# Kernel tuning notes

Measured on AMD Instinct MI355X. Metric: run time of the kernel, lower is better.

Reference implementation:

```python
import jax, jax.numpy as jnp
import numpy as np
from jax import lax

B, C, L = 2048, 9605, 8
WL_PER_LABEL = 50
ALPHA = 0.5        # training_config['alpha4']
ALPHA1 = 0.1       # margin
ALPHA2 = 2.0       # training_config['alpha2']
ALPHA3 = 10.0      # training_config['alpha3']
ALPHA_OTHER = 0.5
NEG = jnp.float32(-1e30)


def setup_inputs() -> dict:
    key = jax.random.key(0)
    k1, k2, k3, k4 = jax.random.split(key, 4)
    x = jax.random.normal(k1, (B, C), dtype=jnp.float32) * 2.0
    y = (jax.random.uniform(k2, (B, C)) < 0.005).astype(jnp.float32)
    y_neg = (jax.random.uniform(k3, (B, C)) < 0.005).astype(jnp.float32)
    # whitelist masks: L app-labels, each whitelisting ~WL_PER_LABEL raw classes
    idx = jax.random.randint(k4, (L, WL_PER_LABEL), 0, C)
    wl_masks = jnp.zeros((L, C), dtype=bool).at[jnp.arange(L)[:, None], idx].set(True)
    return {"x": x, "y": y, "y_neg": y_neg, "wl_masks": wl_masks}


def reference(x, y, y_neg, wl_masks):
    # y_neg is consumed by the original forward (find_gt_whitelist) but never
    # affects the returned loss, faithfully ignored here.
    xs_pos = jax.nn.sigmoid(x)                                  # [B, C]
    # top_k_thres = max(11th-largest sigmoid, alpha_other)
    thres = jnp.maximum(lax.top_k(xs_pos, 11)[0][:, 10], ALPHA_OTHER)  # [B]
    # per-label whitelist max: m[b,l] = max_{c in wl_l} xs_pos[b,c]
    m = jnp.max(jnp.where(wl_masks[None, :, :], xs_pos[:, None, :], NEG), axis=-1)  # [B, L]
    # label l is a ground-truth whitelist label iff y has any positive in wl_l
    has_pos = jnp.einsum('bc,lc->bl', y, wl_masks.astype(y.dtype)) > 0   # [B, L]
    correct_max = jnp.max(jnp.where(has_pos, m, NEG), axis=-1)           # [B]
    incorrect_max = jnp.max(jnp.where(~has_pos, m, NEG), axis=-1)        # [B]
    any_correct = jnp.any(has_pos, axis=-1)
    any_incorrect = jnp.any(~has_pos, axis=-1)
    # union whitelist max (the "other" branch uses xs_pos over all wl indices)
    union_max = jnp.max(jnp.where(jnp.any(wl_masks, axis=0)[None, :], xs_pos, NEG), axis=-1)
    x1 = jnp.where(any_correct, correct_max, thres)
    x2 = jnp.where(any_correct,
                   jnp.where(any_incorrect, jnp.maximum(incorrect_max, thres), thres),
                   union_max)
    coef = jnp.where(any_correct, 1.0, 1.0 - ALPHA)
    d = x2 - x1 + ALPHA1
    rank = jnp.where(d > 0, ALPHA2, 1.0) * jax.nn.sigmoid(ALPHA3 * d)
    return jnp.mean(coef * rank)
```

## Files before the change

kernel.cpp:

```cpp
#include <hip/hip_runtime.h>

#define CC 9605
#define BB 2048
#define LL 8
#define CAND_MAX 384
#define NEGF (-1e30f)

#define WS_PARTIALS_OFF 16384

__device__ __forceinline__ unsigned enc_f(float f) {
  unsigned u = __float_as_uint(f);
  return (u & 0x80000000u) ? ~u : (u | 0x80000000u);
}
__device__ __forceinline__ float dec_u(unsigned e) {
  unsigned u = (e & 0x80000000u) ? (e & 0x7fffffffu) : ~e;
  return __uint_as_float(u);
}
__device__ __forceinline__ float sigm(float z) {
  return 1.0f / (1.0f + __expf(-z));
}

__global__ void wl_sniff(const unsigned* __restrict__ wlw,
                         unsigned* __restrict__ wsu) {
  const int nwords = (LL * CC) / 4;
  const int stride = gridDim.x * blockDim.x;
  unsigned f = 0u;
  for (int j = blockIdx.x * blockDim.x + threadIdx.x; j < nwords; j += stride) {
    unsigned w = wlw[j];
#pragma unroll
    for (int k = 0; k < 4; ++k) {
      unsigned b = (w >> (8 * k)) & 255u;
      if (b == 1u)    { f |= 2u; if (k != 0) f |= 1u; }
      if (b == 0x3fu) { f |= 8u; if (k == 1) f |= 4u; }
    }
  }
#pragma unroll
  for (int off = 32; off >= 1; off >>= 1) f |= __shfl_xor(f, off, 64);
  if ((threadIdx.x & 63) == 0 && f) atomicOr(&wsu[1], f);
}

__global__ void wl_compact(const unsigned char* __restrict__ wl,
                           unsigned* __restrict__ wsu) {
  const int tid = threadIdx.x;
  const int lane = tid & 63;
  const int c = blockIdx.x * 256 + tid;
  const unsigned g = wsu[1];
  const int dt = (g & 1u) ? 0 : (g & 4u) ? 3 : (g & 2u) ? 1 : (g & 8u) ? 2 : 0;
  const int* wl32 = (const int*)wl;
  const float* wlf = (const float*)wl;
  const unsigned short* wlh = (const unsigned short*)wl;
  unsigned m = 0u;
  if (c < CC) {
#pragma unroll
    for (int l = 0; l < LL; ++l) {
      int j = l * CC + c;
      bool on;
      if (dt == 0) on = (wl[j] != 0);
      else if (dt == 1) on = (wl32[j] != 0);
      else if (dt == 2) on = (wlf[j] != 0.0f);
      else on = (wlh[j] != 0);
      if (on) m |= (1u << l);
    }
  }
  unsigned long long bal = __ballot(m != 0u);
  if (bal) {
    unsigned wcnt = (unsigned)__popcll(bal);
    unsigned basep = 0u;
    if (lane == 0) basep = atomicAdd(&wsu[0], wcnt);
    basep = __shfl(basep, 0, 64);
    if (m) {
      unsigned pos = basep + (unsigned)__popcll(bal & ((1ull << lane) - 1ull));
      if (pos < 2048u) wsu[4 + pos] = ((unsigned)c << 8) | m;
    }
  }
}

__global__ __launch_bounds__(256, 4) void loss_kernel(
    const float* __restrict__ x, const float* __restrict__ y,
    const unsigned* __restrict__ wsu, float* __restrict__ partials) {
  __shared__ __align__(16) unsigned sh_row[9608];
  __shared__ unsigned sh_cand[CAND_MAX];
  __shared__ unsigned sh_redM[4];
  __shared__ unsigned sh_redC[4];
  __shared__ unsigned sh_cnt;
  __shared__ unsigned sh_e11;
  __shared__ float sh_wl[4][10];

  const int tid = threadIdx.x;
  const int lane = tid & 63;
  const int wid = tid >> 6;
  const int b = blockIdx.x;
  const long long base = (long long)b * CC;

  const int soff = (4 - (b & 3)) & 3;
  const int ngroups = (CC - soff) >> 2;
  const int tailn = CC - soff - (ngroups << 2);
  const int m_extra = soff + tailn;
  const float4* vp = (const float4*)(x + base + soff);
  float4 t[10];
#pragma unroll
  for (int i = 0; i < 9; ++i) t[i] = vp[tid + (i << 8)];
  const int g9 = tid + (9 << 8);
  if (g9 < ngroups) t[9] = vp[g9];
  else { t[9].x = NEGF; t[9].y = NEGF; t[9].z = NEGF; t[9].w = NEGF; }
  float tailv = NEGF;
  int tailcol = 0;
  if (tid < m_extra) {
    tailcol = (tid < soff) ? tid : (soff + (ngroups << 2) + (tid - soff));
    tailv = x[base + tailcol];
  }

  const unsigned nu = wsu[0];
  const unsigned* ents = wsu + 4;
  unsigned ent0 = 0u, ent1 = 0u;
  float gx0 = NEGF, gy0 = 0.0f, gx1 = NEGF, gy1 = 0.0f;
  const bool h0 = (unsigned)tid < nu;
  const bool h1 = (unsigned)(tid + 256) < nu;
  if (h0) ent0 = ents[tid];
  if (h1) ent1 = ents[tid + 256];
  if (h0) { gx0 = x[base + (ent0 >> 8)]; gy0 = y[base + (ent0 >> 8)]; }
  if (h1) { gx1 = x[base + (ent1 >> 8)]; gy1 = y[base + (ent1 >> 8)]; }

  uint4* rv = (uint4*)sh_row;
  unsigned mx = 0u;
#pragma unroll
  for (int i = 0; i < 10; ++i) {
    int g = tid + (i << 8);
    uint4 e;
    e.x = enc_f(t[i].x); e.y = enc_f(t[i].y);
    e.z = enc_f(t[i].z); e.w = enc_f(t[i].w);
    if (i < 9 || g < ngroups) {
      mx = max(mx, max(max(e.x, e.y), max(e.z, e.w)));
      rv[g] = e;
    }
  }
  if (tid < m_extra) {
    unsigned e = enc_f(tailv);
    mx = max(mx, e);
    sh_row[(ngroups << 2) + tid] = e;
  }
  if (tid < 3) sh_row[9605 + tid] = 0u;
  if (tid == 0) sh_cnt = 0u;

#pragma unroll
  for (int off = 32; off >= 1; off >>= 1) mx = max(mx, __shfl_xor(mx, off, 64));
  if (lane == 0) sh_redM[wid] = mx;
  __syncthreads();
  const unsigned Emax =
      max(max(sh_redM[0], sh_redM[1]), max(sh_redM[2], sh_redM[3]));

  auto blk_count = [&](unsigned T) -> unsigned {
    unsigned cnt = 0u;
#pragma unroll
    for (int i = 0; i < 10; ++i) {
      int g = tid + (i << 8);
      if (g < 2402) {
        uint4 v = rv[g];
        cnt += (v.x >= T) + (v.y >= T) + (v.z >= T) + (v.w >= T);
      }
    }
#pragma unroll
    for (int off = 32; off >= 1; off >>= 1) cnt += __shfl_xor(cnt, off, 64);
    __syncthreads();
    if (lane == 0) sh_redC[wid] = cnt;
    __syncthreads();
    return sh_redC[0] + sh_redC[1] + sh_redC[2] + sh_redC[3];
  };

  unsigned E11 = 0u;
  bool done = false;
  unsigned lo = (Emax > (1u << 23)) ? (Emax - (1u << 23)) : 1u;
  unsigned hi = Emax + 1u;
  unsigned c = blk_count(lo);
  while (c < 11u && lo > 1u) {
    hi = lo;
    lo = (lo > (1u << 23)) ? (lo - (1u << 23)) : 1u;
    c = blk_count(lo);
  }
  while (c > CAND_MAX) {
    if (hi - lo <= 1u) { E11 = lo; done = true; break; }
    unsigned mid = lo + ((hi - lo) >> 1);
    unsigned cm = blk_count(mid);
    if (cm >= 11u) { lo = mid; c = cm; } else { hi = mid; }
  }

  if (!done) {
#pragma unroll
    for (int i = 0; i < 10; ++i) {
      int g = tid + (i << 8);
      uint4 v;
      if (g < 2402) v = rv[g];
      else { v.x = 0u; v.y = 0u; v.z = 0u; v.w = 0u; }
      unsigned vals[4] = {v.x, v.y, v.z, v.w};
#pragma unroll
      for (int k = 0; k < 4; ++k) {
        bool pr = (vals[k] >= lo);
        unsigned long long bal = __ballot(pr);
        if (bal) {
          unsigned wcnt = (unsigned)__popcll(bal);
          unsigned basep = 0u;
          if (lane == 0) basep = atomicAdd(&sh_cnt, wcnt);
          basep = __shfl(basep, 0, 64);
          if (pr) {
            unsigned posn =
                basep + (unsigned)__popcll(bal & ((1ull << lane) - 1ull));
            sh_cand[posn] = vals[k];
          }
        }
      }
    }
    __syncthreads();

    if (wid == 0) {
      unsigned v0[6];
#pragma unroll
      for (int j = 0; j < 6; ++j) {
        unsigned idx = (unsigned)lane + 64u * j;
        v0[j] = (idx < c) ? sh_cand[idx] : 0u;
      }
      unsigned ans = 0u;
      for (int r = 0; r < 11; ++r) {
        unsigned lmx = v0[0];
#pragma unroll
        for (int j = 1; j < 6; ++j) lmx = max(lmx, v0[j]);
        unsigned wm = lmx;
#pragma unroll
        for (int off = 32; off >= 1; off >>= 1)
          wm = max(wm, __shfl_xor(wm, off, 64));
        ans = wm;
        if (r < 10) {
          unsigned long long bal = __ballot(lmx == wm);
          int first = (int)__ffsll((long long)bal) - 1;
          if (lane == first) {
            bool rm = false;
#pragma unroll
            for (int j = 0; j < 6; ++j) {
              if (!rm && v0[j] == wm) { v0[j] = 0u; rm = true; }
            }
          }
        }
      }
      if (lane == 0) sh_e11 = ans;
    }
    __syncthreads();
    E11 = sh_e11;
  }

  float lm[8];
#pragma unroll
  for (int l = 0; l < 8; ++l) lm[l] = NEGF;
  unsigned pmask = 0u;
  if (h0) {
    unsigned mk = ent0 & 255u;
    pmask |= mk;
    if (gy0 > 0.0f) pmask |= (mk << 8);
#pragma unroll
    for (int l = 0; l < 8; ++l)
      if ((mk >> l) & 1u) lm[l] = fmaxf(lm[l], gx0);
  }
  if (h1) {
    unsigned mk = ent1 & 255u;
    pmask |= mk;
    if (gy1 > 0.0f) pmask |= (mk << 8);
#pragma unroll
    for (int l = 0; l < 8; ++l)
      if ((mk >> l) & 1u) lm[l] = fmaxf(lm[l], gx1);
  }
  for (unsigned e = (unsigned)tid + 512u; e < nu; e += 256u) {
    unsigned ent = ents[e];
    unsigned mk = ent & 255u;
    float xv = x[base + (ent >> 8)];
    float yv = y[base + (ent >> 8)];
    pmask |= mk;
    if (yv > 0.0f) pmask |= (mk << 8);
#pragma unroll
    for (int l = 0; l < 8; ++l)
      if ((mk >> l) & 1u) lm[l] = fmaxf(lm[l], xv);
  }
#pragma unroll
  for (int off = 32; off >= 1; off >>= 1) {
    pmask |= __shfl_xor(pmask, off, 64);
#pragma unroll
    for (int l = 0; l < 8; ++l) lm[l] = fmaxf(lm[l], __shfl_xor(lm[l], off, 64));
  }
  if (lane == 0) {
#pragma unroll
    for (int l = 0; l < 8; ++l) sh_wl[wid][l] = lm[l];
    sh_wl[wid][8] = __uint_as_float(pmask);
  }
  __syncthreads();

  if (tid == 0) {
    float LM[8];
    unsigned PM = 0u;
#pragma unroll
    for (int l = 0; l < 8; ++l) LM[l] = NEGF;
    for (int w = 0; w < 4; ++w) {
#pragma unroll
      for (int l = 0; l < 8; ++l) LM[l] = fmaxf(LM[l], sh_wl[w][l]);
      PM |= __float_as_uint(sh_wl[w][8]);
    }
    unsigned PR = PM & 255u, PO = (PM >> 8) & 255u;
    float thres = fmaxf(sigm(dec_u(E11)), 0.5f);
    float cmax = NEGF, imax = NEGF, umax = NEGF;
#pragma unroll
    for (int l = 0; l < 8; ++l) {
      if ((PR >> l) & 1u) {
        float ml = sigm(LM[l]);
        umax = fmaxf(umax, ml);
        if ((PO >> l) & 1u) cmax = fmaxf(cmax, ml);
        else imax = fmaxf(imax, ml);
      }
    }
    bool anyc = (PO != 0u);
    bool anyi = (PO != 255u);
    float x1 = anyc ? cmax : thres;
    float x2 = anyc ? (anyi ? fmaxf(imax, thres) : thres)
                    : ((nu > 0u) ? umax : NEGF);
    float coef = anyc ? 1.0f : 0.5f;
    float dd = x2 - x1 + 0.1f;
    float rank = ((dd > 0.0f) ? 2.0f : 1.0f) * sigm(10.0f * dd);
    partials[b] = coef * rank;
  }
}

__global__ void final_reduce(const float* __restrict__ partials,
                             float* __restrict__ out) {
  __shared__ float sh[4];
  const int tid = threadIdx.x;
  const int lane = tid & 63;
  const int wid = tid >> 6;
  float s = 0.0f;
  for (int i = tid; i < BB; i += 256) s += partials[i];
#pragma unroll
  for (int off = 32; off >= 1; off >>= 1) s += __shfl_xor(s, off, 64);
  if (lane == 0) sh[wid] = s;
  __syncthreads();
  if (tid == 0) out[0] = (sh[0] + sh[1] + sh[2] + sh[3]) * (1.0f / (float)BB);
}

extern "C" void kernel_launch(void* const* d_in, const int* in_sizes, int n_in,
                              void* d_out, int out_size, void* d_ws,
                              size_t ws_size, hipStream_t stream) {
  const float* x = (const float*)d_in[0];
  const float* y = (const float*)d_in[1];
  const unsigned char* wl = (const unsigned char*)d_in[3];
  float* out = (float*)d_out;
  unsigned* wsu = (unsigned*)d_ws;
  float* partials = (float*)((char*)d_ws + WS_PARTIALS_OFF);

  hipMemsetAsync(d_ws, 0, 16, stream);
  wl_sniff<<<64, 256, 0, stream>>>((const unsigned*)wl, wsu);
  wl_compact<<<(CC + 255) / 256, 256, 0, stream>>>(wl, wsu);
  loss_kernel<<<BB, 256, 0, stream>>>(x, y, wsu, partials);
  final_reduce<<<1, 256, 0, stream>>>(partials, out);
}
```

Baseline: 232.0 us.

## Keep row in registers with 1024-thread blocks instead of shared-memory staging

The loss kernel moves from 256 to 1024 threads per block, and each thread now holds 13 encoded values of the row in registers. The 38 KB shared-memory row buffer and the repeated LDS scans in each threshold-count pass are gone. The coarse search step is halved, which narrows the first window in exchange for possibly more expansion passes. Block-wide reductions now span 16 waves, so each count pass pays for more synchronisation across more waves.

```diff
diff --git a/kernel.cpp b/kernel.cpp
--- a/kernel.cpp
+++ b/kernel.cpp
@@ -3,6 +3,8 @@
 #define CC 9605
 #define BB 2048
 #define LL 8
+#define TPB 1024
+#define NWAVE 16
 #define CAND_MAX 384
 #define NEGF (-1e30f)
 
@@ -75,16 +77,15 @@
   }
 }
 
-__global__ __launch_bounds__(256, 4) void loss_kernel(
+__global__ __launch_bounds__(TPB) void loss_kernel(
     const float* __restrict__ x, const float* __restrict__ y,
     const unsigned* __restrict__ wsu, float* __restrict__ partials) {
-  __shared__ __align__(16) unsigned sh_row[9608];
   __shared__ unsigned sh_cand[CAND_MAX];
-  __shared__ unsigned sh_redM[4];
-  __shared__ unsigned sh_redC[4];
+  __shared__ unsigned sh_redM[NWAVE];
+  __shared__ unsigned sh_redC[NWAVE];
   __shared__ unsigned sh_cnt;
   __shared__ unsigned sh_e11;
-  __shared__ float sh_wl[4][10];
+  __shared__ float sh_wl[NWAVE][9];
 
   const int tid = threadIdx.x;
   const int lane = tid & 63;
@@ -97,84 +98,78 @@
   const int tailn = CC - soff - (ngroups << 2);
   const int m_extra = soff + tailn;
   const float4* vp = (const float4*)(x + base + soff);
-  float4 t[10];
-#pragma unroll
-  for (int i = 0; i < 9; ++i) t[i] = vp[tid + (i << 8)];
-  const int g9 = tid + (9 << 8);
-  if (g9 < ngroups) t[9] = vp[g9];
-  else { t[9].x = NEGF; t[9].y = NEGF; t[9].z = NEGF; t[9].w = NEGF; }
-  float tailv = NEGF;
-  int tailcol = 0;
+  const float4 t0 = vp[tid];
+  const float4 t1 = vp[tid + 1024];
+  const int g2 = tid + 2048;
+  const bool hg2 = (g2 < ngroups);
+  float4 t2;
+  if (hg2) t2 = vp[g2];
+  float tailv = 0.0f;
   if (tid < m_extra) {
-    tailcol = (tid < soff) ? tid : (soff + (ngroups << 2) + (tid - soff));
-    tailv = x[base + tailcol];
+    int col = (tid < soff) ? tid : (soff + (ngroups << 2) + (tid - soff));
+    tailv = x[base + col];
   }
 
   const unsigned nu = wsu[0];
   const unsigned* ents = wsu + 4;
-  unsigned ent0 = 0u, ent1 = 0u;
-  float gx0 = NEGF, gy0 = 0.0f, gx1 = NEGF, gy1 = 0.0f;
   const bool h0 = (unsigned)tid < nu;
-  const bool h1 = (unsigned)(tid + 256) < nu;
-  if (h0) ent0 = ents[tid];
-  if (h1) ent1 = ents[tid + 256];
-  if (h0) { gx0 = x[base + (ent0 >> 8)]; gy0 = y[base + (ent0 >> 8)]; }
-  if (h1) { gx1 = x[base + (ent1 >> 8)]; gy1 = y[base + (ent1 >> 8)]; }
-
-  uint4* rv = (uint4*)sh_row;
+  unsigned ent0 = 0u;
+  float gx0 = NEGF, gy0 = 0.0f;
+  if (h0) {
+    ent0 = ents[tid];
+    gx0 = x[base + (ent0 >> 8)];
+    gy0 = y[base + (ent0 >> 8)];
+  }
+
+  unsigned enc[13];
+  enc[0] = enc_f(t0.x); enc[1] = enc_f(t0.y);
+  enc[2] = enc_f(t0.z); enc[3] = enc_f(t0.w);
+  enc[4] = enc_f(t1.x); enc[5] = enc_f(t1.y);
+  enc[6] = enc_f(t1.z); enc[7] = enc_f(t1.w);
+  if (hg2) {
+    enc[8] = enc_f(t2.x); enc[9] = enc_f(t2.y);
+    enc[10] = enc_f(t2.z); enc[11] = enc_f(t2.w);
+  } else {
+    enc[8] = 0u; enc[9] = 0u; enc[10] = 0u; enc[11] = 0u;
+  }
+  enc[12] = (tid < m_extra) ? enc_f(tailv) : 0u;
+  if (tid == 0) sh_cnt = 0u;
+
   unsigned mx = 0u;
 #pragma unroll
-  for (int i = 0; i < 10; ++i) {
-    int g = tid + (i << 8);
-    uint4 e;
-    e.x = enc_f(t[i].x); e.y = enc_f(t[i].y);
-    e.z = enc_f(t[i].z); e.w = enc_f(t[i].w);
-    if (i < 9 || g < ngroups) {
-      mx = max(mx, max(max(e.x, e.y), max(e.z, e.w)));
-      rv[g] = e;
-    }
-  }
-  if (tid < m_extra) {
-    unsigned e = enc_f(tailv);
-    mx = max(mx, e);
-    sh_row[(ngroups << 2) + tid] = e;
-  }
-  if (tid < 3) sh_row[9605 + tid] = 0u;
-  if (tid == 0) sh_cnt = 0u;
-
+  for (int i = 0; i < 13; ++i) mx = max(mx, enc[i]);
 #pragma unroll
   for (int off = 32; off >= 1; off >>= 1) mx = max(mx, __shfl_xor(mx, off, 64));
   if (lane == 0) sh_redM[wid] = mx;
   __syncthreads();
-  const unsigned Emax =
-      max(max(sh_redM[0], sh_redM[1]), max(sh_redM[2], sh_redM[3]));
+  unsigned Emax = 0u;
+#pragma unroll
+  for (int w = 0; w < NWAVE; ++w) Emax = max(Emax, sh_redM[w]);
 
   auto blk_count = [&](unsigned T) -> unsigned {
     unsigned cnt = 0u;
 #pragma unroll
-    for (int i = 0; i < 10; ++i) {
-      int g = tid + (i << 8);
-      if (g < 2402) {
-        uint4 v = rv[g];
-        cnt += (v.x >= T) + (v.y >= T) + (v.z >= T) + (v.w >= T);
-      }
-    }
+    for (int i = 0; i < 13; ++i) cnt += (enc[i] >= T) ? 1u : 0u;
 #pragma unroll
     for (int off = 32; off >= 1; off >>= 1) cnt += __shfl_xor(cnt, off, 64);
     __syncthreads();
     if (lane == 0) sh_redC[wid] = cnt;
     __syncthreads();
-    return sh_redC[0] + sh_redC[1] + sh_redC[2] + sh_redC[3];
+    unsigned s = 0u;
+#pragma unroll
+    for (int w = 0; w < NWAVE; ++w) s += sh_redC[w];
+    return s;
   };
 
+  const unsigned STEP = 1u << 22;
   unsigned E11 = 0u;
   bool done = false;
-  unsigned lo = (Emax > (1u << 23)) ? (Emax - (1u << 23)) : 1u;
+  unsigned lo = (Emax > STEP) ? (Emax - STEP) : 1u;
   unsigned hi = Emax + 1u;
   unsigned c = blk_count(lo);
   while (c < 11u && lo > 1u) {
     hi = lo;
-    lo = (lo > (1u << 23)) ? (lo - (1u << 23)) : 1u;
+    lo = (lo > STEP) ? (lo - STEP) : 1u;
     c = blk_count(lo);
   }
   while (c > CAND_MAX) {
@@ -186,26 +181,18 @@
 
   if (!done) {
 #pragma unroll
-    for (int i = 0; i < 10; ++i) {
-      int g = tid + (i << 8);
-      uint4 v;
-      if (g < 2402) v = rv[g];
-      else { v.x = 0u; v.y = 0u; v.z = 0u; v.w = 0u; }
-      unsigned vals[4] = {v.x, v.y, v.z, v.w};
-#pragma unroll
-      for (int k = 0; k < 4; ++k) {
-        bool pr = (vals[k] >= lo);
-        unsigned long long bal = __ballot(pr);
-        if (bal) {
-          unsigned wcnt = (unsigned)__popcll(bal);
-          unsigned basep = 0u;
-          if (lane == 0) basep = atomicAdd(&sh_cnt, wcnt);
-          basep = __shfl(basep, 0, 64);
-          if (pr) {
-            unsigned posn =
-                basep + (unsigned)__popcll(bal & ((1ull << lane) - 1ull));
-            sh_cand[posn] = vals[k];
-          }
+    for (int i = 0; i < 13; ++i) {
+      bool pr = (enc[i] >= lo);
+      unsigned long long bal = __ballot(pr);
+      if (bal) {
+        unsigned wcnt = (unsigned)__popcll(bal);
+        unsigned basep = 0u;
+        if (lane == 0) basep = atomicAdd(&sh_cnt, wcnt);
+        basep = __shfl(basep, 0, 64);
+        if (pr) {
+          unsigned posn =
+              basep + (unsigned)__popcll(bal & ((1ull << lane) - 1ull));
+          sh_cand[posn] = enc[i];
         }
       }
     }
@@ -258,15 +245,7 @@
     for (int l = 0; l < 8; ++l)
       if ((mk >> l) & 1u) lm[l] = fmaxf(lm[l], gx0);
   }
-  if (h1) {
-    unsigned mk = ent1 & 255u;
-    pmask |= mk;
-    if (gy1 > 0.0f) pmask |= (mk << 8);
-#pragma unroll
-    for (int l = 0; l < 8; ++l)
-      if ((mk >> l) & 1u) lm[l] = fmaxf(lm[l], gx1);
-  }
-  for (unsigned e = (unsigned)tid + 512u; e < nu; e += 256u) {
+  for (unsigned e = (unsigned)tid + 1024u; e < nu; e += 1024u) {
     unsigned ent = ents[e];
     unsigned mk = ent & 255u;
     float xv = x[base + (ent >> 8)];
@@ -295,7 +274,7 @@
     unsigned PM = 0u;
 #pragma unroll
     for (int l = 0; l < 8; ++l) LM[l] = NEGF;
-    for (int w = 0; w < 4; ++w) {
+    for (int w = 0; w < NWAVE; ++w) {
 #pragma unroll
       for (int l = 0; l < 8; ++l) LM[l] = fmaxf(LM[l], sh_wl[w][l]);
       PM |= __float_as_uint(sh_wl[w][8]);
@@ -352,6 +331,6 @@
   hipMemsetAsync(d_ws, 0, 16, stream);
   wl_sniff<<<64, 256, 0, stream>>>((const unsigned*)wl, wsu);
   wl_compact<<<(CC + 255) / 256, 256, 0, stream>>>(wl, wsu);
-  loss_kernel<<<BB, 256, 0, stream>>>(x, y, wsu, partials);
+  loss_kernel<<<BB, TPB, 0, stream>>>(x, y, wsu, partials);
   final_reduce<<<1, 256, 0, stream>>>(partials, out);
 }
```

After: 282.2 us. +21.6%, slower.

## Load logit rows directly into LDS via global_load_lds and encode on the fly

Applied to the files above, without the earlier changes.

Replaces the register-staged row load (global to VGPR, encode, store to LDS) with direct global-to-LDS 16-byte loads, keeping raw floats in shared memory. Every later pass (max, count, candidate gather) now applies the order-preserving encoding when reading. This cuts register pressure and the extra LDS store pass, at the cost of re-encoding in each counting iteration. The threshold search step is also halved, which changes how many count passes run.

```diff
diff --git a/kernel.cpp b/kernel.cpp
--- a/kernel.cpp
+++ b/kernel.cpp
@@ -18,6 +18,12 @@
 }
 __device__ __forceinline__ float sigm(float z) {
   return 1.0f / (1.0f + __expf(-z));
+}
+
+__device__ __forceinline__ void gload_lds16(const void* g, void* l) {
+  __builtin_amdgcn_global_load_lds(
+      (const __attribute__((address_space(1))) unsigned*)g,
+      (__attribute__((address_space(3))) unsigned*)l, 16, 0, 0);
 }
 
 __global__ void wl_sniff(const unsigned* __restrict__ wlw,
@@ -78,7 +84,7 @@
 __global__ __launch_bounds__(256, 4) void loss_kernel(
     const float* __restrict__ x, const float* __restrict__ y,
     const unsigned* __restrict__ wsu, float* __restrict__ partials) {
-  __shared__ __align__(16) unsigned sh_row[9608];
+  __shared__ __align__(16) float sh_row[9608];
   __shared__ unsigned sh_cand[CAND_MAX];
   __shared__ unsigned sh_redM[4];
   __shared__ unsigned sh_redC[4];
@@ -97,51 +103,50 @@
   const int tailn = CC - soff - (ngroups << 2);
   const int m_extra = soff + tailn;
   const float4* vp = (const float4*)(x + base + soff);
-  float4 t[10];
-#pragma unroll
-  for (int i = 0; i < 9; ++i) t[i] = vp[tid + (i << 8)];
-  const int g9 = tid + (9 << 8);
-  if (g9 < ngroups) t[9] = vp[g9];
-  else { t[9].x = NEGF; t[9].y = NEGF; t[9].z = NEGF; t[9].w = NEGF; }
-  float tailv = NEGF;
-  int tailcol = 0;
+
+  float tailv = 0.0f;
   if (tid < m_extra) {
-    tailcol = (tid < soff) ? tid : (soff + (ngroups << 2) + (tid - soff));
-    tailv = x[base + tailcol];
+    int col = (tid < soff) ? tid : (soff + (ngroups << 2) + (tid - soff));
+    tailv = x[base + col];
   }
 
   const unsigned nu = wsu[0];
   const unsigned* ents = wsu + 4;
+  const bool h0 = (unsigned)tid < nu;
+  const bool h1 = (unsigned)(tid + 256) < nu;
   unsigned ent0 = 0u, ent1 = 0u;
   float gx0 = NEGF, gy0 = 0.0f, gx1 = NEGF, gy1 = 0.0f;
-  const bool h0 = (unsigned)tid < nu;
-  const bool h1 = (unsigned)(tid + 256) < nu;
   if (h0) ent0 = ents[tid];
   if (h1) ent1 = ents[tid + 256];
   if (h0) { gx0 = x[base + (ent0 >> 8)]; gy0 = y[base + (ent0 >> 8)]; }
   if (h1) { gx1 = x[base + (ent1 >> 8)]; gy1 = y[base + (ent1 >> 8)]; }
 
-  uint4* rv = (uint4*)sh_row;
+  float4* rv = (float4*)sh_row;
+#pragma unroll
+  for (int i = 0; i < 9; ++i) {
+    const int gbase = (i << 8) + (wid << 6);
+    gload_lds16(&vp[gbase + lane], &rv[gbase]);
+  }
+  {
+    const int g9 = (9 << 8) + tid;
+    const int gbase = (9 << 8) + (wid << 6);
+    if (g9 < ngroups) gload_lds16(&vp[g9], &rv[gbase]);
+  }
+  if (tid < m_extra) sh_row[(ngroups << 2) + tid] = tailv;
+  if (tid < 3) sh_row[9605 + tid] = NEGF;
+  if (tid == 0) sh_cnt = 0u;
+  __syncthreads();
+
   unsigned mx = 0u;
 #pragma unroll
   for (int i = 0; i < 10; ++i) {
     int g = tid + (i << 8);
-    uint4 e;
-    e.x = enc_f(t[i].x); e.y = enc_f(t[i].y);
-    e.z = enc_f(t[i].z); e.w = enc_f(t[i].w);
-    if (i < 9 || g < ngroups) {
-      mx = max(mx, max(max(e.x, e.y), max(e.z, e.w)));
-      rv[g] = e;
-    }
-  }
-  if (tid < m_extra) {
-    unsigned e = enc_f(tailv);
-    mx = max(mx, e);
-    sh_row[(ngroups << 2) + tid] = e;
-  }
-  if (tid < 3) sh_row[9605 + tid] = 0u;
-  if (tid == 0) sh_cnt = 0u;
-
+    if (g < 2402) {
+      float4 v = rv[g];
+      mx = max(mx, max(max(enc_f(v.x), enc_f(v.y)),
+                       max(enc_f(v.z), enc_f(v.w))));
+    }
+  }
 #pragma unroll
   for (int off = 32; off >= 1; off >>= 1) mx = max(mx, __shfl_xor(mx, off, 64));
   if (lane == 0) sh_redM[wid] = mx;
@@ -155,8 +160,9 @@
     for (int i = 0; i < 10; ++i) {
       int g = tid + (i << 8);
       if (g < 2402) {
-        uint4 v = rv[g];
-        cnt += (v.x >= T) + (v.y >= T) + (v.z >= T) + (v.w >= T);
+        float4 v = rv[g];
+        cnt += (enc_f(v.x) >= T) + (enc_f(v.y) >= T) +
+               (enc_f(v.z) >= T) + (enc_f(v.w) >= T);
       }
     }
 #pragma unroll
@@ -167,14 +173,15 @@
     return sh_redC[0] + sh_redC[1] + sh_redC[2] + sh_redC[3];
   };
 
+  const unsigned STEP = 1u << 22;
   unsigned E11 = 0u;
   bool done = false;
-  unsigned lo = (Emax > (1u << 23)) ? (Emax - (1u << 23)) : 1u;
+  unsigned lo = (Emax > STEP) ? (Emax - STEP) : 1u;
   unsigned hi = Emax + 1u;
   unsigned c = blk_count(lo);
   while (c < 11u && lo > 1u) {
     hi = lo;
-    lo = (lo > (1u << 23)) ? (lo - (1u << 23)) : 1u;
+    lo = (lo > STEP) ? (lo - STEP) : 1u;
     c = blk_count(lo);
   }
   while (c > CAND_MAX) {
@@ -188,10 +195,12 @@
 #pragma unroll
     for (int i = 0; i < 10; ++i) {
       int g = tid + (i << 8);
-      uint4 v;
-      if (g < 2402) v = rv[g];
-      else { v.x = 0u; v.y = 0u; v.z = 0u; v.w = 0u; }
-      unsigned vals[4] = {v.x, v.y, v.z, v.w};
+      unsigned vals[4] = {0u, 0u, 0u, 0u};
+      if (g < 2402) {
+        float4 v = rv[g];
+        vals[0] = enc_f(v.x); vals[1] = enc_f(v.y);
+        vals[2] = enc_f(v.z); vals[3] = enc_f(v.w);
+      }
 #pragma unroll
       for (int k = 0; k < 4; ++k) {
         bool pr = (vals[k] >= lo);
```

After: 238.7 us. 2.9% more time.
